# Kernel tuning notes

Hardware: AMD Instinct MI355X
Metric: run time of the kernel (lower is better)

The kernel has to match this reference:

```python
import jax, jax.numpy as jnp
from jax import lax
import numpy as np

KS = 15          # dark-channel window
PAD = (KS - 1) // 2
TEMP = 10000.0   # positional encoding temperature
NPF = 32         # max(num_pos_feats_x, y, z)
EPS = 1e-6


def _conv1x1(x, w, b):
    # x: [B,C,H,W], w: [O,C], b: [O]
    return jnp.einsum('bchw,oc->bohw', x, w) + b[None, :, None, None]


def _conv2s2(x, w, b):
    # kernel 2, stride 2, no padding; w: [O,I,2,2]
    y = lax.conv_general_dilated(x, w, (2, 2), 'VALID',
                                 dimension_numbers=('NCHW', 'OIHW', 'NCHW'))
    return y + b[None, :, None, None]


def _lrelu(x):
    return jnp.where(x >= 0, x, 0.1 * x)


def _resize(x, h, w):
    return jax.image.resize(x, (x.shape[0], x.shape[1], h, w), method='bilinear')


def _dark_channel(x):
    # min over channels, reflect pad, 15x15 sliding min (== unfold+min in torch)
    dm = jnp.min(x, axis=1, keepdims=True)  # [B,1,H,W]
    dm = jnp.pad(dm, ((0, 0), (0, 0), (PAD, PAD), (PAD, PAD)), mode='reflect')
    return lax.reduce_window(dm, jnp.inf, lax.min,
                             (1, 1, KS, KS), (1, 1, 1, 1), 'VALID')


def _sincos(e, d, dim_t):
    # e: [B,H,W] -> [B,H,W,d] with interleaved sin/cos (torch stack+flatten)
    p = e[..., None] / dim_t[:d]
    return jnp.stack((jnp.sin(p[..., 0::2]), jnp.cos(p[..., 1::2])),
                     axis=4).reshape(e.shape + (d,))


def _pos_encoding(x, dark):
    B, _, H, W = x.shape
    scale = 2.0 * np.pi
    yv = jnp.arange(H, dtype=jnp.float32)
    xv = jnp.arange(W, dtype=jnp.float32)
    ye = jnp.broadcast_to((yv / (yv[-1] + EPS) * scale)[None, :, None], (B, H, W))
    xe = jnp.broadcast_to((xv / (xv[-1] + EPS) * scale)[None, None, :], (B, H, W))
    z = dark[:, 0]
    ze = z / (jnp.max(z, axis=(1, 2), keepdims=True) + EPS) * scale
    dim_t = TEMP ** (2.0 * (jnp.arange(NPF, dtype=jnp.float32) // 2) / NPF)
    pos_x = _sincos(xe, 16, dim_t)
    pos_y = _sincos(ye, 16, dim_t)
    pos_z = _sincos(ze, 32, dim_t)
    return jnp.concatenate((pos_x, pos_y, pos_z), axis=3).transpose(0, 3, 1, 2)


def _forward(x, w_cf1, b_cf1, w_e1, b_e1, w_e2, b_e2, w_d1, b_d1, w_d2, b_d2,
             w_pha1, b_pha1, w_pha2, b_pha2, w_amp1, b_amp1, w_amp2, b_amp2,
             w_spat1, b_spat1, w_spat2, b_spat2, w_u1, b_u1, w_u2, b_u2,
             w_u3, b_u3, w_u4, b_u4, w_cf2, b_cf2, w_cf3, b_cf3):
    xori = x
    dark = _dark_channel(1.0 - x)            # DCP of inverted image [B,1,512,512]
    ape = _pos_encoding(x, dark) + _conv1x1(x, w_cf1, b_cf1)  # [B,64,H,W]

    x_f = _conv1x1(_conv1x1(x, w_e1, b_e1), w_e2, b_e2)       # [B,64,512,512]
    x_d1 = _conv2s2(x_f, w_d1, b_d1)                          # [B,128,256,256]
    x_d2 = _conv2s2(x_d1, w_d2, b_d2)                         # [B,256,128,128]
    Hd, Wd = x_d2.shape[2], x_d2.shape[3]

    x_freq = jnp.fft.rfft2(x_d2)             # norm='backward' (default)
    x_pha = jnp.angle(x_freq)
    x_amp = jnp.abs(x_freq)
    # phase branch is computed but unused downstream (matches original code)
    x_pha = _conv1x1(_lrelu(_conv1x1(x_pha, w_pha1, b_pha1)), w_pha2, b_pha2)
    x_amp = _conv1x1(_lrelu(_conv1x1(x_amp, w_amp1, b_amp1)), w_amp2, b_amp2)
    x_four = jnp.fft.irfft2(lax.complex(x_amp * jnp.cos(x_amp),
                                        x_amp * jnp.sin(x_amp)), s=(Hd, Wd))
    x_four = _conv1x1(_resize(x_four, x_d1.shape[2], x_d1.shape[3]), w_u1, b_u1)
    x_four = _conv1x1(_resize(x_four, x_f.shape[2], x_f.shape[3]), w_u2, b_u2)

    x_spat = _conv1x1(_lrelu(_conv1x1(x_d2, w_spat1, b_spat1)), w_spat2, b_spat2)
    x_spat = _conv1x1(_resize(x_spat, x_d1.shape[2], x_d1.shape[3]), w_u3, b_u3)
    x_spat = _conv1x1(_resize(x_spat, x_f.shape[2], x_f.shape[3]), w_u4, b_u4)
    x_spat = x_spat * ape

    four_spa = jnp.concatenate((x_four, x_spat), axis=1)      # [B,128,512,512]
    out = _conv1x1(_conv1x1(four_spa, w_cf2, b_cf2), w_cf3, b_cf3)
    return out + xori


def setup_inputs() -> dict:
    key = jax.random.key(0)
    ks = iter(jax.random.split(key, 64))
    def W(*shape):
        return 0.02 * jax.random.normal(next(ks), shape, dtype=jnp.float32)
    def Bb(n):
        return 0.01 * jax.random.normal(next(ks), (n,), dtype=jnp.float32)
    nc = 64
    inp = {'x': jax.random.uniform(next(ks), (1, 3, 512, 512), dtype=jnp.float32)}
    inp.update(w_cf1=W(nc, 3), b_cf1=Bb(nc))
    inp.update(w_e1=W(nc // 8, 3), b_e1=Bb(nc // 8))
    inp.update(w_e2=W(nc, nc // 8), b_e2=Bb(nc))
    inp.update(w_d1=W(2 * nc, nc, 2, 2), b_d1=Bb(2 * nc))
    inp.update(w_d2=W(4 * nc, 2 * nc, 2, 2), b_d2=Bb(4 * nc))
    for nm in ('pha', 'amp', 'spat'):
        inp['w_%s1' % nm] = W(4 * nc, 4 * nc); inp['b_%s1' % nm] = Bb(4 * nc)
        inp['w_%s2' % nm] = W(4 * nc, 4 * nc); inp['b_%s2' % nm] = Bb(4 * nc)
    inp.update(w_u1=W(2 * nc, 4 * nc), b_u1=Bb(2 * nc))
    inp.update(w_u2=W(nc, 2 * nc), b_u2=Bb(nc))
    inp.update(w_u3=W(2 * nc, 4 * nc), b_u3=Bb(2 * nc))
    inp.update(w_u4=W(nc, 2 * nc), b_u4=Bb(nc))
    inp.update(w_cf2=W(nc, 2 * nc), b_cf2=Bb(nc))
    inp.update(w_cf3=W(3, nc), b_cf3=Bb(3))
    return inp


def reference(x, w_cf1, b_cf1, w_e1, b_e1, w_e2, b_e2, w_d1, b_d1, w_d2, b_d2,
              w_pha1, b_pha1, w_pha2, b_pha2, w_amp1, b_amp1, w_amp2, b_amp2,
              w_spat1, b_spat1, w_spat2, b_spat2, w_u1, b_u1, w_u2, b_u2,
              w_u3, b_u3, w_u4, b_u4, w_cf2, b_cf2, w_cf3, b_cf3):
    return _forward(x, w_cf1, b_cf1, w_e1, b_e1, w_e2, b_e2, w_d1, b_d1,
                    w_d2, b_d2, w_pha1, b_pha1, w_pha2, b_pha2, w_amp1, b_amp1,
                    w_amp2, b_amp2, w_spat1, b_spat1, w_spat2, b_spat2,
                    w_u1, b_u1, w_u2, b_u2, w_u3, b_u3, w_u4, b_u4,
                    w_cf2, b_cf2, w_cf3, b_cf3)
```

## Files before the change

### kernel.cpp

```cpp
#include <hip/hip_runtime.h>
#include <math.h>

#define PI_F 3.14159265358979323846f
#define NPIX 262144

typedef __attribute__((ext_vector_type(8))) short sh8;
typedef __attribute__((ext_vector_type(4))) float fx4;
typedef __attribute__((ext_vector_type(4))) unsigned short ush4;

__device__ __forceinline__ unsigned short f2bf(float v) {
    unsigned u = __float_as_uint(v);
    return (unsigned short)((u + 0x7FFFu + ((u >> 16) & 1)) >> 16);
}
__device__ __forceinline__ float bf2f(unsigned short h) {
    return __uint_as_float((unsigned)h << 16);
}

__device__ __forceinline__ int refl512(int t) {
    if (t < 0) t = -t;
    if (t > 511) t = 1022 - t;
    return t;
}

__device__ __forceinline__ void prep_one(const float* __restrict__ w, unsigned short* __restrict__ h,
                                         unsigned short* __restrict__ l, int N, int K, int cshift, int idx) {
    if (idx >= N * K) return;
    int n = idx / K, kord = idx - n * K;
    int ksrc = kord;
    if (cshift) {
        int dydx = kord >> cshift, c = kord & ((1 << cshift) - 1);
        ksrc = c * 4 + dydx;
    }
    float v = w[n * K + ksrc];
    unsigned short hb = f2bf(v);
    h[idx] = hb;
    if (l) l[idx] = f2bf(v - bf2f(hb));
}

__global__ __launch_bounds__(256) void k_prep(
    const float* __restrict__ x, float* __restrict__ dark, float* __restrict__ blockmax,
    const float* __restrict__ w_d2, unsigned short* __restrict__ d2h, unsigned short* __restrict__ d2l,
    const float* __restrict__ w_a1, unsigned short* __restrict__ a1h, unsigned short* __restrict__ a1l,
    const float* __restrict__ w_a2, unsigned short* __restrict__ a2h, unsigned short* __restrict__ a2l,
    const float* __restrict__ w_s1, unsigned short* __restrict__ s1h,
    unsigned short* __restrict__ BfH, unsigned short* __restrict__ BfL,
    unsigned short* __restrict__ BfcH, unsigned short* __restrict__ BfcL,
    unsigned short* __restrict__ BicH, unsigned short* __restrict__ BicL,
    float* __restrict__ Birf, float* __restrict__ zbias,
    const float* __restrict__ w_e1, const float* __restrict__ b_e1,
    const float* __restrict__ w_e2, const float* __restrict__ b_e2,
    const float* __restrict__ w_d1, const float* __restrict__ b_d1,
    unsigned short* __restrict__ d1ch, float* __restrict__ b1c,
    const float* __restrict__ w_u3, const float* __restrict__ w_u4,
    const float* __restrict__ b_u3, const float* __restrict__ b_u4,
    const float* __restrict__ wsp2, const float* __restrict__ bsp2,
    unsigned short* __restrict__ Wg, float* __restrict__ bgc,
    const float* __restrict__ w2, const float* __restrict__ b2,
    const float* __restrict__ w3, const float* __restrict__ b3,
    const float* __restrict__ wu2, const float* __restrict__ bu2,
    const float* __restrict__ wu1, const float* __restrict__ bu1,
    float* __restrict__ Wc, float* __restrict__ bc,
    float* __restrict__ W21c, float* __restrict__ b21c) {
    __shared__ float smem[8448];
    int b = blockIdx.x, tid = threadIdx.x;
    if (b < 512)       { prep_one(w_d2, d2h, d2l, 256, 512, 7, b * 256 + tid); return; }
    else if (b < 768)  { prep_one(w_a1, a1h, a1l, 256, 256, 0, (b - 512) * 256 + tid); return; }
    else if (b < 1024) { prep_one(w_a2, a2h, a2l, 256, 256, 0, (b - 768) * 256 + tid); return; }
    else if (b < 1280) { prep_one(w_s1, s1h, nullptr, 256, 256, 0, (b - 1024) * 256 + tid); return; }
    else if (b < 2000) {
        int idx = (b - 1280) * 256 + tid;
        if (idx < 256) zbias[idx] = 0.f;
        const float w0 = 2.f * PI_F / 128.f;
        float v;
        unsigned short *H, *L;
        int off;
        if (idx < 32768) {
            int n = idx >> 7, k = idx & 127;
            int t = n & 127, r = (t * k) & 127;
            float s_, c_; sincosf(w0 * r, &s_, &c_);
            v = (n < 128) ? c_ : -s_;
            H = BfH; L = BfL; off = idx;
        } else if (idx < 98304) {
            int i = idx - 32768;
            int n = i >> 8, j = i & 255;
            int t = n & 127, r = (t * (j & 127)) & 127;
            float s_, c_; sincosf(w0 * r, &s_, &c_);
            v = (n < 128) ? ((j < 128) ? c_ : s_) : ((j < 128) ? -s_ : c_);
            H = BfcH; L = BfcL; off = i;
        } else if (idx < 163840) {
            int i = idx - 98304;
            int n = i >> 8, j = i & 255;
            int t = n & 127, r = (t * (j & 127)) & 127;
            float s_, c_; sincosf(w0 * r, &s_, &c_);
            v = ((n < 128) ? ((j < 128) ? c_ : -s_) : ((j < 128) ? s_ : c_)) * (1.f / 128.f);
            H = BicH; L = BicL; off = i;
        } else if (idx < 184320) {
            int i2 = idx - 163840;
            int col = i2 / 160, j = i2 - col * 160;
            if (j == 0) v = 1.f / 128.f;
            else if (j < 64)  { int r = (j * col) & 127; float s_, c_; sincosf(w0 * r, &s_, &c_); v = 2.f * c_ / 128.f; }
            else if (j == 64) v = (col & 1) ? -1.f / 128.f : 1.f / 128.f;
            else if (j >= 66 && j <= 128) { int k = j - 65; int r = (k * col) & 127; float s_, c_; sincosf(w0 * r, &s_, &c_); v = -2.f * s_ / 128.f; }
            else v = 0.f;
            Birf[j * 128 + col] = v;
            return;
        } else return;
        unsigned short hb = f2bf(v);
        H[off] = hb;
        L[off] = f2bf(v - bf2f(hb));
    }
    else if (b < 2016) {
        float* E = smem;
        if (tid < 192) {
            int o = tid / 3, ci = tid - o * 3;
            float s = 0.f;
            #pragma unroll
            for (int r = 0; r < 8; r++) s += w_e2[o * 8 + r] * w_e1[r * 3 + ci];
            E[tid] = s;
        }
        __syncthreads();
        int idx = (b - 2000) * 256 + tid;
        int n = idx >> 5, k = idx & 31;
        float s = 0.f;
        if (k < 12) {
            int dydx = k / 3, ci = k - dydx * 3;
            #pragma unroll 16
            for (int o = 0; o < 64; o++) s += w_d1[n * 256 + o * 4 + dydx] * E[o * 3 + ci];
        }
        d1ch[idx] = f2bf(s);
    } else if (b == 2016) {
        float* f = smem;
        if (tid < 64) {
            int o = tid;
            float s = b_e2[o];
            #pragma unroll
            for (int r = 0; r < 8; r++) s += w_e2[o * 8 + r] * b_e1[r];
            f[o] = s;
        }
        __syncthreads();
        if (tid < 128) {
            float s = b_d1[tid];
            #pragma unroll 8
            for (int o = 0; o < 64; o++) {
                float fo = f[o];
                #pragma unroll
                for (int dydx = 0; dydx < 4; dydx++) s += w_d1[tid * 256 + o * 4 + dydx] * fo;
            }
            b1c[tid] = s;
        }
    } else if (b == 2017) {
        float* sWc = smem;
        float* sW2c = smem + 384;
        if (tid < 128) {
            int j = tid;
            for (int r = 0; r < 3; r++) {
                float s = 0.f;
                #pragma unroll 16
                for (int o = 0; o < 64; o++) s += w3[r * 64 + o] * w2[o * 128 + j];
                sWc[r * 128 + j] = s;
                Wc[r * 128 + j] = s;
            }
            if (j < 3) {
                float s = b3[j];
                #pragma unroll 16
                for (int o = 0; o < 64; o++) s += w3[j * 64 + o] * b2[o];
                bc[j] = s;
            }
        }
        __syncthreads();
        if (tid < 128) {
            int j = tid;
            for (int r = 0; r < 3; r++) {
                float s = 0.f;
                #pragma unroll 16
                for (int o = 0; o < 64; o++) s += sWc[r * 128 + o] * wu2[o * 128 + j];
                sW2c[r * 128 + j] = s;
            }
        }
        __syncthreads();
        if (tid < 256) {
            int j = tid;
            for (int r = 0; r < 3; r++) {
                float s = 0.f;
                #pragma unroll 16
                for (int o = 0; o < 128; o++) s += sW2c[r * 128 + o] * wu1[o * 256 + j];
                W21c[r * 256 + j] = s;
            }
        }
        if (tid < 3) {
            float s = 0.f;
            #pragma unroll 16
            for (int o = 0; o < 128; o++) s += sW2c[tid * 128 + o] * bu1[o];
            #pragma unroll 16
            for (int o = 0; o < 64; o++)  s += sWc[tid * 128 + o] * bu2[o];
            b21c[tid] = s;
        }
    } else if (b < 2082) {
        int n = b - 2018;
        float* u = smem;
        float* red = smem + 256;
        {
            float s = 0.f;
            #pragma unroll 16
            for (int o = 0; o < 128; o++) s += w_u4[n * 128 + o] * w_u3[o * 256 + tid];
            u[tid] = s;
        }
        __syncthreads();
        float s = 0.f;
        #pragma unroll 16
        for (int o = 0; o < 256; o++) s += u[o] * wsp2[o * 256 + tid];
        Wg[n * 256 + tid] = f2bf(s);
        float rv = u[tid] * bsp2[tid];
        if (tid < 128) rv += w_u4[n * 128 + tid] * b_u3[tid];
        red[tid] = rv;
        __syncthreads();
        for (int st = 128; st > 0; st >>= 1) {
            if (tid < st) red[tid] += red[tid + st];
            __syncthreads();
        }
        if (tid == 0) bgc[n] = b_u4[n] + red[0];
    } else {
        int i = b - 2082;
        float* rm = smem;
        float* cm = smem + 7680;
        float* red = smem + 8192;
        for (int idx = tid; idx < 15 * 512; idx += 256) {
            int rr = idx >> 9, j = idx & 511;
            int row = refl512(i - 7 + rr);
            int p = (row << 9) + j;
            rm[rr * 512 + j] = 1.0f - fmaxf(x[p], fmaxf(x[p + NPIX], x[p + 2 * NPIX]));
        }
        __syncthreads();
        #pragma unroll
        for (int h = 0; h < 2; h++) {
            int j = tid + h * 256;
            float m = 1e30f;
            #pragma unroll
            for (int rr = 0; rr < 15; rr++) m = fminf(m, rm[rr * 512 + j]);
            cm[j] = m;
        }
        __syncthreads();
        float best = -1e30f;
        #pragma unroll
        for (int h = 0; h < 2; h++) {
            int j = tid + h * 256;
            float m = 1e30f;
            #pragma unroll
            for (int d = -7; d <= 7; d++) m = fminf(m, cm[refl512(j + d)]);
            dark[(i << 9) + j] = m;
            best = fmaxf(best, m);
        }
        red[tid] = best;
        __syncthreads();
        for (int s = 128; s > 0; s >>= 1) {
            if (tid < s) red[tid] = fmaxf(red[tid], red[tid + s]);
            __syncthreads();
        }
        if (tid == 0) blockmax[i] = red[0];
    }
}

template<int AMODE, int SPLIT, int LRELU, int TSTORE, int ABF16, int CBF16>
__device__ __forceinline__ void mm_body(unsigned short* __restrict__ SH,
                                        const void* __restrict__ Asrc_,
                                        const unsigned short* __restrict__ Bh,
                                        const unsigned short* __restrict__ Bl,
                                        const float* __restrict__ bias, void* __restrict__ C_,
                                        int M, int N, int K, int cshift, int wshift, int srcW,
                                        int gy, int bid, int nwg) {
    const float* Af = (const float*)Asrc_;
    const unsigned short* A16 = (const unsigned short*)Asrc_;
    float* Cf = (float*)C_;
    unsigned short* C16 = (unsigned short*)C_;
    unsigned short* AhS = SH;
    unsigned short* BhS = SH + 5120;
    unsigned short* AlS = SPLIT ? SH + 7680 : SH;
    unsigned short* BlS = SPLIT ? SH + 12800 : SH;
    int tid = threadIdx.x;
    int qq = nwg >> 3, rr = nwg & 7;
    int xcd = bid & 7, ixw = bid >> 3;
    int work = (xcd < rr) ? (xcd * (qq + 1) + ixw) : (rr * (qq + 1) + (xcd - rr) * qq + ixw);
    int bx = work / gy;
    int by = work - bx * gy;
    int m0 = bx * 128;
    int n0 = by * 64;
    int wave = tid >> 6, lane = tid & 63;
    int wm = (wave >> 1) * 64, wn = (wave & 1) * 32;
    int l15 = lane & 15, quad = lane >> 4;
    int lk = quad * 8, lk4 = quad * 4;
    fx4 acc[4][2];
    #pragma unroll
    for (int a = 0; a < 4; a++)
        #pragma unroll
        for (int b = 0; b < 2; b++)
            acc[a][b] = (fx4){0.f, 0.f, 0.f, 0.f};

    int mm = tid & 127;
    int kpb = tid >> 7;
    int gm = m0 + mm;
    int oj = 0, oi = 0, cA = 0, kfA = 0;
    size_t abase = 0;
    if (AMODE == 1) { oj = gm & ((1 << wshift) - 1); oi = gm >> wshift; }
    if (AMODE == 2) { oj = gm & 255; oi = gm >> 8; }
    if (AMODE == 3) abase = (size_t)gm * K;
    if (AMODE == 7) { cA = gm / 65; kfA = gm - cA * 65; }
    if (AMODE == 9) { cA = gm / 65; kfA = gm - cA * 65; }

    for (int kb = 0; kb < K; kb += 32) {
        if (AMODE == 3 && ABF16 && !SPLIT) {
            #pragma unroll
            for (int half = 0; half < 2; half++) {
                sh8 hv = *(const sh8*)(const void*)&A16[abase + kb + kpb * 16 + half * 8];
                *(sh8*)(void*)&AhS[mm * 40 + (kpb * 2 + half) * 8] = hv;
            }
        } else {
            #pragma unroll
            for (int half = 0; half < 2; half++) {
                sh8 hv, lv;
                #pragma unroll
                for (int tt = 0; tt < 4; tt++) {
                    int kp = kpb * 8 + half * 4 + tt;
                    int k0 = kb + kp * 2;
                    unsigned short h0, h1;
                    if (ABF16) {
                        size_t ad0, ad1;
                        if (AMODE == 0) {
                            ad0 = (size_t)k0 * M + gm;
                            ad1 = ad0 + M;
                        } else if (AMODE == 1) {
                            int c = k0 & ((1 << cshift) - 1);
                            int dydx = k0 >> cshift;
                            int dy = dydx >> 1, dx = dydx & 1;
                            size_t pix = (size_t)(2 * oi + dy) * srcW + (2 * oj + dx);
                            size_t plane = (size_t)srcW * srcW;
                            ad0 = (size_t)c * plane + pix;
                            ad1 = ad0 + plane;
                        } else if (AMODE == 3) {
                            ad0 = abase + k0;
                            ad1 = ad0 + 1;
                        } else {
                            int t0 = k0 & 127, hf = k0 >> 7;
                            ad0 = (size_t)(cA * 128 + t0) * 256 + hf * 128 + kfA;
                            ad1 = ad0 + 256;
                        }
                        h0 = A16[ad0];
                        h1 = A16[ad1];
                    } else {
                        float a0, a1;
                        if (AMODE == 2) {
                            if (k0 < 12) {
                                int d0 = k0 / 3, c0 = k0 - d0 * 3;
                                int k1 = k0 + 1;
                                int d1x = k1 / 3, c1 = k1 - d1x * 3;
                                a0 = Af[(size_t)c0 * NPIX + (size_t)(2 * oi + (d0 >> 1)) * 512 + 2 * oj + (d0 & 1)];
                                a1 = Af[(size_t)c1 * NPIX + (size_t)(2 * oi + (d1x >> 1)) * 512 + 2 * oj + (d1x & 1)];
                            } else { a0 = 0.f; a1 = 0.f; }
                        } else if (AMODE == 9) {
                            size_t ad = (size_t)cA * 16640 + (size_t)k0 * 65 + kfA;
                            float re0 = Af[ad], im0 = Af[ad + 2129920];
                            float re1 = Af[ad + 65], im1 = Af[ad + 65 + 2129920];
                            a0 = sqrtf(re0 * re0 + im0 * im0);
                            a1 = sqrtf(re1 * re1 + im1 * im1);
                        } else {
                            size_t ad0 = (size_t)k0 * M + gm;
                            a0 = Af[ad0];
                            a1 = Af[ad0 + M];
                        }
                        h0 = f2bf(a0);
                        h1 = f2bf(a1);
                        if (SPLIT) {
                            lv[tt * 2] = (short)f2bf(a0 - bf2f(h0));
                            lv[tt * 2 + 1] = (short)f2bf(a1 - bf2f(h1));
                        }
                    }
                    hv[tt * 2] = (short)h0;
                    hv[tt * 2 + 1] = (short)h1;
                }
                int coff = (kpb * 2 + half) * 8;
                *(sh8*)(void*)&AhS[mm * 40 + coff] = hv;
                if (SPLIT) *(sh8*)(void*)&AlS[mm * 40 + coff] = lv;
            }
        }
        {
            int n = tid >> 2, seg = tid & 3;
            size_t gb = (size_t)(n0 + n) * K + kb + seg * 8;
            *(sh8*)(void*)&BhS[n * 40 + seg * 8] = *(const sh8*)(const void*)&Bh[gb];
            if (SPLIT) *(sh8*)(void*)&BlS[n * 40 + seg * 8] = *(const sh8*)(const void*)&Bl[gb];
        }
        __syncthreads();
        sh8 af[4], bf[2], afl[4], bfl[2];
        #pragma unroll
        for (int mt = 0; mt < 4; mt++) {
            af[mt] = *(const sh8*)(const void*)&AhS[(wm + mt * 16 + l15) * 40 + lk];
            if (SPLIT) afl[mt] = *(const sh8*)(const void*)&AlS[(wm + mt * 16 + l15) * 40 + lk];
        }
        #pragma unroll
        for (int nt = 0; nt < 2; nt++) {
            bf[nt] = *(const sh8*)(const void*)&BhS[(wn + nt * 16 + l15) * 40 + lk];
            if (SPLIT) bfl[nt] = *(const sh8*)(const void*)&BlS[(wn + nt * 16 + l15) * 40 + lk];
        }
        #pragma unroll
        for (int mt = 0; mt < 4; mt++)
            #pragma unroll
            for (int nt = 0; nt < 2; nt++) {
                acc[mt][nt] = __builtin_amdgcn_mfma_f32_16x16x32_bf16(af[mt], bf[nt], acc[mt][nt], 0, 0, 0);
                if (SPLIT) {
                    acc[mt][nt] = __builtin_amdgcn_mfma_f32_16x16x32_bf16(af[mt], bfl[nt], acc[mt][nt], 0, 0, 0);
                    acc[mt][nt] = __builtin_amdgcn_mfma_f32_16x16x32_bf16(afl[mt], bf[nt], acc[mt][nt], 0, 0, 0);
                }
            }
        __syncthreads();
    }
    #pragma unroll
    for (int nt = 0; nt < 2; nt++) {
        int n = n0 + wn + nt * 16 + l15;
        float bs = bias[n];
        #pragma unroll
        for (int mt = 0; mt < 4; mt++) {
            int mbase = m0 + wm + mt * 16 + lk4;
            if (TSTORE) {
                #pragma unroll
                for (int r = 0; r < 4; r++) {
                    float q = acc[mt][nt][r] + bs;
                    if (LRELU) q = (q < 0.f) ? 0.1f * q : q;
                    if (CBF16) C16[(size_t)(mbase + r) * N + n] = f2bf(q);
                    else       Cf[(size_t)(mbase + r) * N + n] = q;
                }
            } else if (CBF16) {
                ush4 v;
                #pragma unroll
                for (int r = 0; r < 4; r++) {
                    float q = acc[mt][nt][r] + bs;
                    if (LRELU) q = (q < 0.f) ? 0.1f * q : q;
                    v[r] = f2bf(q);
                }
                *(ush4*)(void*)&C16[(size_t)n * M + mbase] = v;
            } else {
                float4 v;
                float* vp = (float*)&v;
                #pragma unroll
                for (int r = 0; r < 4; r++) {
                    float q = acc[mt][nt][r] + bs;
                    if (LRELU) q = (q < 0.f) ? 0.1f * q : q;
                    vp[r] = q;
                }
                *(float4*)&Cf[(size_t)n * M + mbase] = v;
            }
        }
    }
}

template<int AMODE, int SPLIT, int LRELU, int TSTORE, int ABF16, int CBF16>
__global__ __launch_bounds__(256) void k_mmcf(const void* __restrict__ Asrc_,
                                              const unsigned short* __restrict__ Bh,
                                              const unsigned short* __restrict__ Bl,
                                              const float* __restrict__ bias, void* __restrict__ C_,
                                              int M, int N, int K, int cshift, int wshift, int srcW,
                                              int gy) {
    __shared__ unsigned short SH[SPLIT ? 15360 : 7680];
    mm_body<AMODE, SPLIT, LRELU, TSTORE, ABF16, CBF16>(SH, Asrc_, Bh, Bl, bias, C_,
                                                       M, N, K, cshift, wshift, srcW, gy,
                                                       (int)blockIdx.x, (int)gridDim.x);
}

__global__ __launch_bounds__(256) void k_d1(const float* __restrict__ x,
                                            const unsigned short* __restrict__ d1ch,
                                            const float* __restrict__ b1c, unsigned short* __restrict__ xd1,
                                            const float* __restrict__ blockmax, int* __restrict__ gmax) {
    if (blockIdx.x == 1024) {
        __shared__ float red[256];
        int tid = threadIdx.x;
        red[tid] = fmaxf(blockmax[tid], blockmax[tid + 256]);
        __syncthreads();
        for (int s = 128; s > 0; s >>= 1) {
            if (tid < s) red[tid] = fmaxf(red[tid], red[tid + s]);
            __syncthreads();
        }
        if (tid == 0) gmax[0] = __float_as_int(red[0]);
        return;
    }
    __shared__ unsigned short SH[7680];
    mm_body<2, 0, 0, 0, 0, 1>(SH, x, d1ch, nullptr, b1c, xd1, 65536, 128, 32, 0, 0, 0, 2,
                              (int)blockIdx.x, 1024);
}

__global__ __launch_bounds__(256) void k_dualA(const unsigned short* __restrict__ xd2,
                                               const unsigned short* __restrict__ BfH,
                                               const float* __restrict__ zbias, unsigned short* __restrict__ F1T,
                                               const unsigned short* __restrict__ s1h,
                                               const float* __restrict__ b_sp1, unsigned short* __restrict__ s1) {
    __shared__ unsigned short SH[7680];
    if (blockIdx.x < 1024)
        mm_body<3, 0, 0, 1, 1, 1>(SH, xd2, BfH, nullptr, zbias, F1T, 32768, 256, 128, 0, 0, 0, 4,
                                  (int)blockIdx.x, 1024);
    else
        mm_body<0, 0, 1, 0, 1, 1>(SH, xd2, s1h, nullptr, b_sp1, s1, 16384, 256, 256, 0, 0, 0, 4,
                                  (int)blockIdx.x - 1024, 512);
}

__global__ __launch_bounds__(256) void k_dualB(const unsigned short* __restrict__ F1T,
                                               const unsigned short* __restrict__ BfcH,
                                               const float* __restrict__ zbias, float* __restrict__ F2C,
                                               const unsigned short* __restrict__ s1,
                                               const unsigned short* __restrict__ Wg,
                                               const float* __restrict__ bgc, float* __restrict__ g4s) {
    __shared__ unsigned short SH[7680];
    if (blockIdx.x < 520)
        mm_body<7, 0, 0, 0, 1, 0>(SH, F1T, BfcH, nullptr, zbias, F2C, 16640, 256, 256, 0, 0, 0, 4,
                                  (int)blockIdx.x, 520);
    else
        mm_body<0, 0, 0, 0, 1, 0>(SH, s1, Wg, nullptr, bgc, g4s, 16384, 64, 256, 0, 0, 0, 1,
                                  (int)blockIdx.x - 520, 128);
}

__global__ __launch_bounds__(256) void k_zbuild(const float* __restrict__ A2, unsigned short* __restrict__ Z) {
    int idx = blockIdx.x * 256 + threadIdx.x;
    int ct = idx / 65, kf = idx - ct * 65;
    int c = ct >> 7, t = ct & 127;
    float a = A2[idx];
    float s_, c_;
    sincosf(a, &s_, &c_);
    size_t m = (size_t)c * 65 + kf;
    Z[(size_t)t * 16640 + m] = f2bf(a * c_);
    Z[2129920 + (size_t)t * 16640 + m] = f2bf(a * s_);
}

__global__ __launch_bounds__(256) void k_pfold(const unsigned short* __restrict__ I1T,
                                               const float* __restrict__ W21c, float* __restrict__ P) {
    __shared__ float wa[768];
    int kf = blockIdx.x, tid = threadIdx.x;
    for (int t = tid; t < 768; t += 256) wa[t] = W21c[t];
    __syncthreads();
    float a0 = 0.f, a1 = 0.f, a2 = 0.f;
    #pragma unroll 4
    for (int c = 0; c < 256; c++) {
        float v = bf2f(I1T[(size_t)(c * 65 + kf) * 256 + tid]);
        a0 += wa[c] * v;
        a1 += wa[256 + c] * v;
        a2 += wa[512 + c] * v;
    }
    P[(size_t)(0 * 65 + kf) * 256 + tid] = a0;
    P[(size_t)(1 * 65 + kf) * 256 + tid] = a1;
    P[(size_t)(2 * 65 + kf) * 256 + tid] = a2;
}

__global__ __launch_bounds__(128) void k_h3f(const float* __restrict__ P, const float* __restrict__ Birf,
                                             const float* __restrict__ b21c, float* __restrict__ h3s) {
    __shared__ float sp[390];
    __shared__ float bs[3];
    int tau = blockIdx.x, col = threadIdx.x;
    for (int t = col; t < 390; t += 128) {
        int r = t / 130, rem = t - r * 130;
        int hf = rem / 65, kf = rem - hf * 65;
        sp[t] = P[(size_t)(r * 65 + kf) * 256 + hf * 128 + tau];
    }
    if (col < 3) bs[col] = b21c[col];
    __syncthreads();
    float f0 = 0.f, f1 = 0.f, f2 = 0.f;
    for (int k0 = 0; k0 < 130; k0++) {
        float w = Birf[k0 * 128 + col];
        int hf = (k0 >= 65) ? 1 : 0;
        int base = hf ? (65 + k0 - 65) : k0;
        f0 += w * sp[base];
        f1 += w * sp[130 + base];
        f2 += w * sp[260 + base];
    }
    size_t q = (size_t)tau * 128 + col;
    h3s[q]         = f0 + bs[0];
    h3s[16384 + q] = f1 + bs[1];
    h3s[32768 + q] = f2 + bs[2];
}

__global__ __launch_bounds__(256) void k_final(const float* __restrict__ x,
                                               const float* __restrict__ dark, const int* __restrict__ gmax,
                                               const float* __restrict__ wcf1, const float* __restrict__ bcf1,
                                               const float* __restrict__ Wc, const float* __restrict__ bc,
                                               const float* __restrict__ g4s, const float* __restrict__ h3s,
                                               float* __restrict__ out) {
    __shared__ float idimt[32], w1[192], b1[64], wb[192], bcs[3], posy[16];
    __shared__ float gyr[64][68];
    __shared__ float hyr[3][68];
    int tid = threadIdx.x;
    int bid = blockIdx.x;
    int i = bid >> 1;
    int j0 = (bid & 1) << 8;
    int j = j0 + tid;
    int p = (i << 9) + j;

    const float scale = 2.f * PI_F;
    float inv511 = scale / (511.f + 1e-6f);
    float ye = (float)i * inv511;

    if (tid < 32) idimt[tid] = 1.f / powf(10000.f, (float)(2 * (tid >> 1)) / 32.f);
    if (tid < 192) w1[tid] = wcf1[tid];
    if (tid < 64) b1[tid] = bcf1[tid];
    if (tid < 192) { int r = tid / 64, c = tid - (tid / 64) * 64; wb[tid] = Wc[r * 128 + 64 + c]; }
    if (tid < 3) bcs[tid] = bc[tid];
    __syncthreads();
    if (tid >= 32 && tid < 48) {
        int c = tid - 32;
        float e = ye * idimt[c];
        posy[c] = ((c & 1) == 0) ? __sinf(e) : __cosf(e);
    }

    int ky = i >> 2, ry = i & 3;
    int ym = (ky > 0) ? ky - 1 : 0, yp = (ky < 127) ? ky + 1 : 127;
    float wy0 = (ry == 0) ? .375f : (ry == 1) ? .1875f : (ry == 2) ? .0625f : 0.f;
    float wy1 = (ry == 0 || ry == 3) ? .625f : .75f;
    float wy2 = (ry == 0) ? 0.f : (ry == 1) ? .0625f : (ry == 2) ? .1875f : .375f;
    int base = j0 >> 2;
    int r0 = ym * 128, r1 = ky * 128, r2 = yp * 128;
    for (int idx = tid; idx < 64 * 66; idx += 256) {
        int c = idx / 66, t = idx - c * 66;
        int col = base - 1 + t;
        col = (col < 0) ? 0 : (col > 127) ? 127 : col;
        const float* gp = g4s + (size_t)c * 16384;
        gyr[c][t] = wy0 * gp[r0 + col] + wy1 * gp[r1 + col] + wy2 * gp[r2 + col];
    }
    for (int idx = tid; idx < 3 * 66; idx += 256) {
        int c = idx / 66, t = idx - c * 66;
        int col = base - 1 + t;
        col = (col < 0) ? 0 : (col > 127) ? 127 : col;
        const float* hp = h3s + (size_t)c * 16384;
        hyr[c][t] = wy0 * hp[r0 + col] + wy1 * hp[r1 + col] + wy2 * hp[r2 + col];
    }
    __syncthreads();

    float xe = (float)j * inv511;
    float gm = __int_as_float(gmax[0]);
    float ze = dark[p] / (gm + 1e-6f) * scale;
    float x0 = x[p], x1 = x[p + NPIX], x2 = x[p + 2 * NPIX];

    int rx = j & 3;
    int tx = tid >> 2;
    float wx0 = (rx == 0) ? .375f : (rx == 1) ? .1875f : (rx == 2) ? .0625f : 0.f;
    float wx1 = (rx == 0 || rx == 3) ? .625f : .75f;
    float wx2 = (rx == 0) ? 0.f : (rx == 1) ? .0625f : (rx == 2) ? .1875f : .375f;

    float a0 = 0.f, a1 = 0.f, a2 = 0.f;
    #pragma unroll 1
    for (int c = 0; c < 64; c++) {
        float pos;
        if (c < 16)      { float e = xe * idimt[c];      pos = ((c & 1) == 0) ? __sinf(e) : __cosf(e); }
        else if (c < 32) { pos = posy[c - 16]; }
        else             { float e = ze * idimt[c - 32]; pos = ((c & 1) == 0) ? __sinf(e) : __cosf(e); }
        float ape = pos + w1[c * 3] * x0 + w1[c * 3 + 1] * x1 + w1[c * 3 + 2] * x2 + b1[c];
        float gv = wx0 * gyr[c][tx] + wx1 * gyr[c][tx + 1] + wx2 * gyr[c][tx + 2];
        float s = gv * ape;
        a0 += wb[c] * s; a1 += wb[64 + c] * s; a2 += wb[128 + c] * s;
    }
    float f0 = wx0 * hyr[0][tx] + wx1 * hyr[0][tx + 1] + wx2 * hyr[0][tx + 2];
    float f1 = wx0 * hyr[1][tx] + wx1 * hyr[1][tx + 1] + wx2 * hyr[1][tx + 2];
    float f2 = wx0 * hyr[2][tx] + wx1 * hyr[2][tx + 1] + wx2 * hyr[2][tx + 2];
    out[p]            = a0 + f0 + bcs[0] + x0;
    out[NPIX + p]     = a1 + f1 + bcs[1] + x1;
    out[2 * NPIX + p] = a2 + f2 + bcs[2] + x2;
}

extern "C" void kernel_launch(void* const* d_in, const int* in_sizes, int n_in,
                              void* d_out, int out_size, void* d_ws, size_t ws_size,
                              hipStream_t stream) {
    const float* x      = (const float*)d_in[0];
    const float* w_cf1  = (const float*)d_in[1];  const float* b_cf1 = (const float*)d_in[2];
    const float* w_e1   = (const float*)d_in[3];  const float* b_e1  = (const float*)d_in[4];
    const float* w_e2   = (const float*)d_in[5];  const float* b_e2  = (const float*)d_in[6];
    const float* w_d1   = (const float*)d_in[7];  const float* b_d1  = (const float*)d_in[8];
    const float* w_d2   = (const float*)d_in[9];  const float* b_d2  = (const float*)d_in[10];
    const float* w_amp1 = (const float*)d_in[15]; const float* b_amp1 = (const float*)d_in[16];
    const float* w_amp2 = (const float*)d_in[17]; const float* b_amp2 = (const float*)d_in[18];
    const float* w_sp1  = (const float*)d_in[19]; const float* b_sp1  = (const float*)d_in[20];
    const float* w_sp2  = (const float*)d_in[21]; const float* b_sp2  = (const float*)d_in[22];
    const float* w_u1   = (const float*)d_in[23]; const float* b_u1   = (const float*)d_in[24];
    const float* w_u2   = (const float*)d_in[25]; const float* b_u2   = (const float*)d_in[26];
    const float* w_u3   = (const float*)d_in[27]; const float* b_u3   = (const float*)d_in[28];
    const float* w_u4   = (const float*)d_in[29]; const float* b_u4   = (const float*)d_in[30];
    const float* w_cf2  = (const float*)d_in[31]; const float* b_cf2  = (const float*)d_in[32];
    const float* w_cf3  = (const float*)d_in[33]; const float* b_cf3  = (const float*)d_in[34];
    float* out = (float*)d_out;

    char* ws = (char*)d_ws;
    constexpr size_t MiB = 1ull << 20;
    float*  dark   = (float*)(ws + 0 * MiB);
    int*    gmax   = (int*)  (ws + 2 * MiB);
    float*  Wc     = (float*)(ws + 2 * MiB + 1024);
    float*  bc     = (float*)(ws + 2 * MiB + 2560);
    float*  W21c   = (float*)(ws + 2 * MiB + 4096);
    float*  b21c   = (float*)(ws + 2 * MiB + 7168);
    float*  blockmax = (float*)(ws + 2 * MiB + 8192);
    unsigned short* d1ch = (unsigned short*)(ws + 3 * MiB);
    float*  b1c    = (float*)(ws + 3 * MiB + 16384);
    unsigned short* Wg = (unsigned short*)(ws + 3 * MiB + 131072);
    float*  bgc    = (float*)(ws + 3 * MiB + 196608);
    unsigned short* xd1 = (unsigned short*)(ws + 67 * MiB);
    unsigned short* xd2 = (unsigned short*)(ws + 99 * MiB);
    unsigned short* F1T = (unsigned short*)(ws + 115 * MiB);
    float*  F2C    = (float*)(ws + 147 * MiB);
    float*  A1     = (float*)(ws + 173 * MiB);
    float*  A2     = (float*)(ws + 182 * MiB);
    unsigned short* Zbuf = (unsigned short*)(ws + 115 * MiB);
    unsigned short* I1T  = (unsigned short*)(ws + 132 * MiB);
    float*  P      = (float*)(ws + 149 * MiB);
    float*  h3s    = (float*)(ws + 11 * MiB);
    unsigned short* s1 = (unsigned short*)(ws + 31 * MiB);
    float*  g4s    = (float*)(ws + 87 * MiB);
    unsigned short* wb16 = (unsigned short*)(ws + 192 * MiB);
    unsigned short* d2h = wb16 + 65536,   * d2l = wb16 + 196608;
    unsigned short* a1h = wb16 + 327680,  * a1l = wb16 + 393216;
    unsigned short* a2h = wb16 + 458752,  * a2l = wb16 + 524288;
    unsigned short* s1h = wb16 + 589824;
    unsigned short* BfH = wb16 + 786432,  * BfL = wb16 + 819200;
    unsigned short* BfcH = wb16 + 851968, * BfcL = wb16 + 917504;
    unsigned short* BicH = wb16 + 983040, * BicL = wb16 + 1048576;
    float* zbias = (float*)(ws + 195 * MiB + 512 * 1024);
    float* Birf  = (float*)(ws + 196 * MiB);

    k_prep<<<2594, 256, 0, stream>>>(
        x, dark, blockmax,
        w_d2, d2h, d2l, w_amp1, a1h, a1l, w_amp2, a2h, a2l, w_sp1, s1h,
        BfH, BfL, BfcH, BfcL, BicH, BicL, Birf, zbias,
        w_e1, b_e1, w_e2, b_e2, w_d1, b_d1, d1ch, b1c,
        w_u3, w_u4, b_u3, b_u4, w_sp2, b_sp2, Wg, bgc,
        w_cf2, b_cf2, w_cf3, b_cf3, w_u2, b_u2, w_u1, b_u1,
        Wc, bc, W21c, b21c);

    k_d1<<<1025, 256, 0, stream>>>(x, d1ch, b1c, xd1, blockmax, gmax);
    k_mmcf<1, 0, 0, 0, 1, 1><<<512, 256, 0, stream>>>(xd1, d2h, nullptr, b_d2, xd2, 16384, 256, 512, 7, 7, 256, 4);

    k_dualA<<<1536, 256, 0, stream>>>(xd2, BfH, zbias, F1T, s1h, b_sp1, s1);
    k_dualB<<<648, 256, 0, stream>>>(F1T, BfcH, zbias, F2C, s1, Wg, bgc, g4s);

    k_mmcf<9, 1, 1, 0, 0, 0><<<260, 256, 0, stream>>>(F2C, a1h, a1l, b_amp1, A1, 8320, 256, 256, 0, 0, 0, 4);
    k_mmcf<0, 1, 0, 0, 0, 0><<<260, 256, 0, stream>>>(A1, a2h, a2l, b_amp2, A2, 8320, 256, 256, 0, 0, 0, 4);
    k_zbuild<<<8320, 256, 0, stream>>>(A2, Zbuf);
    k_mmcf<0, 0, 0, 1, 1, 1><<<520, 256, 0, stream>>>(Zbuf, BicH, nullptr, zbias, I1T, 16640, 256, 256, 0, 0, 0, 4);

    k_pfold<<<65, 256, 0, stream>>>(I1T, W21c, P);
    k_h3f<<<128, 128, 0, stream>>>(P, Birf, b21c, h3s);

    k_final<<<1024, 256, 0, stream>>>(x, dark, gmax, w_cf1, b_cf1, Wc, bc, g4s, h3s, out);
}
```

Measured before the change: 314.4 us.

## Fuse zbuild into amp2 GEMM epilogue and merge pfold into h3 kernel

The sincos polar-to-complex build (k_zbuild) moves into the epilogue of the amp2 GEMM, which now writes the bf16 real and imaginary Z buffers directly and no longer makes an fp32 A2 round trip. The channel-fold kernel k_pfold is merged into the h3 kernel, so each block computes only the P values it needs straight from I1T. That removes two launches and two intermediate buffers. In exchange the GEMM epilogue gains scattered 2-byte stores, and the merged h3 kernel does the 256-channel fold with strided global reads across only 128 blocks, which may be slower per block.

```diff
diff --git a/kernel.cpp b/kernel.cpp
--- a/kernel.cpp
+++ b/kernel.cpp
@@ -260,7 +260,7 @@
     }
 }
 
-template<int AMODE, int SPLIT, int LRELU, int TSTORE, int ABF16, int CBF16>
+template<int AMODE, int SPLIT, int LRELU, int TSTORE, int ABF16, int CBF16, int ZOUT>
 __device__ __forceinline__ void mm_body(unsigned short* __restrict__ SH,
                                         const void* __restrict__ Asrc_,
                                         const unsigned short* __restrict__ Bh,
@@ -418,7 +418,19 @@
         #pragma unroll
         for (int mt = 0; mt < 4; mt++) {
             int mbase = m0 + wm + mt * 16 + lk4;
-            if (TSTORE) {
+            if (ZOUT) {
+                #pragma unroll
+                for (int r = 0; r < 4; r++) {
+                    float q = acc[mt][nt][r] + bs;
+                    float s_, c_;
+                    sincosf(q, &s_, &c_);
+                    int m = mbase + r;
+                    int t = m / 65, kf = m - t * 65;
+                    size_t zi = (size_t)t * 16640 + (size_t)n * 65 + kf;
+                    C16[zi] = f2bf(q * c_);
+                    C16[2129920 + zi] = f2bf(q * s_);
+                }
+            } else if (TSTORE) {
                 #pragma unroll
                 for (int r = 0; r < 4; r++) {
                     float q = acc[mt][nt][r] + bs;
@@ -450,7 +462,7 @@
     }
 }
 
-template<int AMODE, int SPLIT, int LRELU, int TSTORE, int ABF16, int CBF16>
+template<int AMODE, int SPLIT, int LRELU, int TSTORE, int ABF16, int CBF16, int ZOUT>
 __global__ __launch_bounds__(256) void k_mmcf(const void* __restrict__ Asrc_,
                                               const unsigned short* __restrict__ Bh,
                                               const unsigned short* __restrict__ Bl,
@@ -458,9 +470,9 @@
                                               int M, int N, int K, int cshift, int wshift, int srcW,
                                               int gy) {
     __shared__ unsigned short SH[SPLIT ? 15360 : 7680];
-    mm_body<AMODE, SPLIT, LRELU, TSTORE, ABF16, CBF16>(SH, Asrc_, Bh, Bl, bias, C_,
-                                                       M, N, K, cshift, wshift, srcW, gy,
-                                                       (int)blockIdx.x, (int)gridDim.x);
+    mm_body<AMODE, SPLIT, LRELU, TSTORE, ABF16, CBF16, ZOUT>(SH, Asrc_, Bh, Bl, bias, C_,
+                                                             M, N, K, cshift, wshift, srcW, gy,
+                                                             (int)blockIdx.x, (int)gridDim.x);
 }
 
 __global__ __launch_bounds__(256) void k_d1(const float* __restrict__ x,
@@ -480,8 +492,8 @@
         return;
     }
     __shared__ unsigned short SH[7680];
-    mm_body<2, 0, 0, 0, 0, 1>(SH, x, d1ch, nullptr, b1c, xd1, 65536, 128, 32, 0, 0, 0, 2,
-                              (int)blockIdx.x, 1024);
+    mm_body<2, 0, 0, 0, 0, 1, 0>(SH, x, d1ch, nullptr, b1c, xd1, 65536, 128, 32, 0, 0, 0, 2,
+                                 (int)blockIdx.x, 1024);
 }
 
 __global__ __launch_bounds__(256) void k_dualA(const unsigned short* __restrict__ xd2,
@@ -491,11 +503,11 @@
                                                const float* __restrict__ b_sp1, unsigned short* __restrict__ s1) {
     __shared__ unsigned short SH[7680];
     if (blockIdx.x < 1024)
-        mm_body<3, 0, 0, 1, 1, 1>(SH, xd2, BfH, nullptr, zbias, F1T, 32768, 256, 128, 0, 0, 0, 4,
-                                  (int)blockIdx.x, 1024);
+        mm_body<3, 0, 0, 1, 1, 1, 0>(SH, xd2, BfH, nullptr, zbias, F1T, 32768, 256, 128, 0, 0, 0, 4,
+                                     (int)blockIdx.x, 1024);
     else
-        mm_body<0, 0, 1, 0, 1, 1>(SH, xd2, s1h, nullptr, b_sp1, s1, 16384, 256, 256, 0, 0, 0, 4,
-                                  (int)blockIdx.x - 1024, 512);
+        mm_body<0, 0, 1, 0, 1, 1, 0>(SH, xd2, s1h, nullptr, b_sp1, s1, 16384, 256, 256, 0, 0, 0, 4,
+                                     (int)blockIdx.x - 1024, 512);
 }
 
 __global__ __launch_bounds__(256) void k_dualB(const unsigned short* __restrict__ F1T,
@@ -506,64 +518,40 @@
                                                const float* __restrict__ bgc, float* __restrict__ g4s) {
     __shared__ unsigned short SH[7680];
     if (blockIdx.x < 520)
-        mm_body<7, 0, 0, 0, 1, 0>(SH, F1T, BfcH, nullptr, zbias, F2C, 16640, 256, 256, 0, 0, 0, 4,
-                                  (int)blockIdx.x, 520);
+        mm_body<7, 0, 0, 0, 1, 0, 0>(SH, F1T, BfcH, nullptr, zbias, F2C, 16640, 256, 256, 0, 0, 0, 4,
+                                     (int)blockIdx.x, 520);
     else
-        mm_body<0, 0, 0, 0, 1, 0>(SH, s1, Wg, nullptr, bgc, g4s, 16384, 64, 256, 0, 0, 0, 1,
-                                  (int)blockIdx.x - 520, 128);
-}
-
-__global__ __launch_bounds__(256) void k_zbuild(const float* __restrict__ A2, unsigned short* __restrict__ Z) {
-    int idx = blockIdx.x * 256 + threadIdx.x;
-    int ct = idx / 65, kf = idx - ct * 65;
-    int c = ct >> 7, t = ct & 127;
-    float a = A2[idx];
-    float s_, c_;
-    sincosf(a, &s_, &c_);
-    size_t m = (size_t)c * 65 + kf;
-    Z[(size_t)t * 16640 + m] = f2bf(a * c_);
-    Z[2129920 + (size_t)t * 16640 + m] = f2bf(a * s_);
-}
-
-__global__ __launch_bounds__(256) void k_pfold(const unsigned short* __restrict__ I1T,
-                                               const float* __restrict__ W21c, float* __restrict__ P) {
-    __shared__ float wa[768];
-    int kf = blockIdx.x, tid = threadIdx.x;
-    for (int t = tid; t < 768; t += 256) wa[t] = W21c[t];
+        mm_body<0, 0, 0, 0, 1, 0, 0>(SH, s1, Wg, nullptr, bgc, g4s, 16384, 64, 256, 0, 0, 0, 1,
+                                     (int)blockIdx.x - 520, 128);
+}
+
+__global__ __launch_bounds__(128) void k_h3m(const unsigned short* __restrict__ I1T,
+                                             const float* __restrict__ W21c, const float* __restrict__ Birf,
+                                             const float* __restrict__ b21c, float* __restrict__ h3s) {
+    __shared__ float wa[768], sp[390], bs[3];
+    int tau = blockIdx.x, col = threadIdx.x;
+    for (int t = col; t < 768; t += 128) wa[t] = W21c[t];
+    if (col < 3) bs[col] = b21c[col];
     __syncthreads();
-    float a0 = 0.f, a1 = 0.f, a2 = 0.f;
-    #pragma unroll 4
-    for (int c = 0; c < 256; c++) {
-        float v = bf2f(I1T[(size_t)(c * 65 + kf) * 256 + tid]);
-        a0 += wa[c] * v;
-        a1 += wa[256 + c] * v;
-        a2 += wa[512 + c] * v;
-    }
-    P[(size_t)(0 * 65 + kf) * 256 + tid] = a0;
-    P[(size_t)(1 * 65 + kf) * 256 + tid] = a1;
-    P[(size_t)(2 * 65 + kf) * 256 + tid] = a2;
-}
-
-__global__ __launch_bounds__(128) void k_h3f(const float* __restrict__ P, const float* __restrict__ Birf,
-                                             const float* __restrict__ b21c, float* __restrict__ h3s) {
-    __shared__ float sp[390];
-    __shared__ float bs[3];
-    int tau = blockIdx.x, col = threadIdx.x;
-    for (int t = col; t < 390; t += 128) {
-        int r = t / 130, rem = t - r * 130;
-        int hf = rem / 65, kf = rem - hf * 65;
-        sp[t] = P[(size_t)(r * 65 + kf) * 256 + hf * 128 + tau];
-    }
-    if (col < 3) bs[col] = b21c[col];
+    for (int pr = col; pr < 130; pr += 128) {
+        int hf = pr / 65, kf = pr - hf * 65;
+        float a0 = 0.f, a1 = 0.f, a2 = 0.f;
+        #pragma unroll 4
+        for (int c = 0; c < 256; c++) {
+            float v = bf2f(I1T[(size_t)(c * 65 + kf) * 256 + hf * 128 + tau]);
+            a0 += wa[c] * v;
+            a1 += wa[256 + c] * v;
+            a2 += wa[512 + c] * v;
+        }
+        sp[pr] = a0; sp[130 + pr] = a1; sp[260 + pr] = a2;
+    }
     __syncthreads();
     float f0 = 0.f, f1 = 0.f, f2 = 0.f;
     for (int k0 = 0; k0 < 130; k0++) {
         float w = Birf[k0 * 128 + col];
-        int hf = (k0 >= 65) ? 1 : 0;
-        int base = hf ? (65 + k0 - 65) : k0;
-        f0 += w * sp[base];
-        f1 += w * sp[130 + base];
-        f2 += w * sp[260 + base];
+        f0 += w * sp[k0];
+        f1 += w * sp[130 + k0];
+        f2 += w * sp[260 + k0];
     }
     size_t q = (size_t)tau * 128 + col;
     h3s[q]         = f0 + bs[0];
@@ -696,10 +684,8 @@
     unsigned short* F1T = (unsigned short*)(ws + 115 * MiB);
     float*  F2C    = (float*)(ws + 147 * MiB);
     float*  A1     = (float*)(ws + 173 * MiB);
-    float*  A2     = (float*)(ws + 182 * MiB);
     unsigned short* Zbuf = (unsigned short*)(ws + 115 * MiB);
     unsigned short* I1T  = (unsigned short*)(ws + 132 * MiB);
-    float*  P      = (float*)(ws + 149 * MiB);
     float*  h3s    = (float*)(ws + 11 * MiB);
     unsigned short* s1 = (unsigned short*)(ws + 31 * MiB);
     float*  g4s    = (float*)(ws + 87 * MiB);
@@ -724,18 +710,16 @@
         Wc, bc, W21c, b21c);
 
     k_d1<<<1025, 256, 0, stream>>>(x, d1ch, b1c, xd1, blockmax, gmax);
-    k_mmcf<1, 0, 0, 0, 1, 1><<<512, 256, 0, stream>>>(xd1, d2h, nullptr, b_d2, xd2, 16384, 256, 512, 7, 7, 256, 4);
+    k_mmcf<1, 0, 0, 0, 1, 1, 0><<<512, 256, 0, stream>>>(xd1, d2h, nullptr, b_d2, xd2, 16384, 256, 512, 7, 7, 256, 4);
 
     k_dualA<<<1536, 256, 0, stream>>>(xd2, BfH, zbias, F1T, s1h, b_sp1, s1);
     k_dualB<<<648, 256, 0, stream>>>(F1T, BfcH, zbias, F2C, s1, Wg, bgc, g4s);
 
-    k_mmcf<9, 1, 1, 0, 0, 0><<<260, 256, 0, stream>>>(F2C, a1h, a1l, b_amp1, A1, 8320, 256, 256, 0, 0, 0, 4);
-    k_mmcf<0, 1, 0, 0, 0, 0><<<260, 256, 0, stream>>>(A1, a2h, a2l, b_amp2, A2, 8320, 256, 256, 0, 0, 0, 4);
-    k_zbuild<<<8320, 256, 0, stream>>>(A2, Zbuf);
-    k_mmcf<0, 0, 0, 1, 1, 1><<<520, 256, 0, stream>>>(Zbuf, BicH, nullptr, zbias, I1T, 16640, 256, 256, 0, 0, 0, 4);
-
-    k_pfold<<<65, 256, 0, stream>>>(I1T, W21c, P);
-    k_h3f<<<128, 128, 0, stream>>>(P, Birf, b21c, h3s);
+    k_mmcf<9, 1, 1, 0, 0, 0, 0><<<260, 256, 0, stream>>>(F2C, a1h, a1l, b_amp1, A1, 8320, 256, 256, 0, 0, 0, 4);
+    k_mmcf<0, 1, 0, 0, 0, 0, 1><<<260, 256, 0, stream>>>(A1, a2h, a2l, b_amp2, Zbuf, 8320, 256, 256, 0, 0, 0, 4);
+    k_mmcf<0, 0, 0, 1, 1, 1, 0><<<520, 256, 0, stream>>>(Zbuf, BicH, nullptr, zbias, I1T, 16640, 256, 256, 0, 0, 0, 4);
+
+    k_h3m<<<128, 128, 0, stream>>>(I1T, W21c, Birf, b21c, h3s);
 
     k_final<<<1024, 256, 0, stream>>>(x, dark, gmax, w_cf1, b_cf1, Wc, bc, g4s, h3s, out);
 }
```

Result: slower. 352.5 us (+12.1%).
